# Optimization experiments

Measured on AMD Instinct MI355X. Metric: run time of the kernel, lower is better.

## Reference

```python
import jax, jax.numpy as jnp
import numpy as np

N = 100_000      # nodes
E = 1_600_000    # edges
F_IN = 128       # node_features
H1, H2 = 50, 20  # GCLSTM hidden sizes (fixed in the model)


def _norm_weights(src, dst, w, n):
    # PyG get_laplacian(sym): remove self loops, deg over row, sym-normalize.
    w = jnp.where(src == dst, jnp.zeros_like(w), w)  # remove self-loops (weight 0)
    deg = jax.ops.segment_sum(w, src, num_segments=n)
    deg_safe = jnp.where(deg > 0, deg, jnp.ones_like(deg))
    dis = jnp.where(deg > 0, deg_safe ** -0.5, jnp.zeros_like(deg))
    return dis[src] * w * dis[dst]


def _lhat_matvec(x, src, dst, wn, n):
    # L_hat = 2*L/lambda_max - I with sym norm and lambda_max=2  =>  -D^-1/2 A D^-1/2
    return -jax.ops.segment_sum(wn[:, None] * x[src], dst, num_segments=n)


def _gclstm_cell(x, src, dst, wn, n, Wx, bx, theta, bconv, out_ch):
    # One GCLSTM step with H = C = 0 (the model passes H=C=None).
    H = jnp.zeros((n, out_ch), x.dtype)
    C = jnp.zeros((n, out_ch), x.dtype)
    # ChebConv(H) for all 4 gates: Tx_0 = H, Tx_1 = L_hat @ H   (K = 2)
    Tx = jnp.stack([H, _lhat_matvec(H, src, dst, wn, n)])       # [2, n, out]
    conv = jnp.einsum('knf,gkfo->gno', Tx, theta) + bconv[:, None, :]  # [4, n, out]
    Z = x @ Wx + bx                                              # [n, 4*out], gates i,f,c,o
    zi, zf, zc, zo = jnp.split(Z, 4, axis=-1)
    I = jax.nn.sigmoid(zi + conv[0])
    Fg = jax.nn.sigmoid(zf + conv[1])
    T = jnp.tanh(zc + conv[2])
    C = Fg * C + I * T
    O = jax.nn.sigmoid(zo + conv[3])
    return O * jnp.tanh(C)


def setup_inputs() -> dict:
    key = jax.random.key(0)
    ks = jax.random.split(key, 14)
    s = 0.1  # param init scale
    return {
        'x': jax.random.normal(ks[0], (N, F_IN), jnp.float32),
        'edge_index': jax.random.randint(ks[1], (2, E), 0, N, dtype=jnp.int32),
        'edge_weight': jax.random.uniform(ks[2], (E,), jnp.float32),
        # layer 1: W_x for gates i,f,c,o concatenated, Cheb thetas [gate, K, in, out]
        'Wx1': s * jax.random.normal(ks[3], (F_IN, 4 * H1), jnp.float32),
        'bx1': s * jax.random.normal(ks[4], (4 * H1,), jnp.float32),
        'theta1': s * jax.random.normal(ks[5], (4, 2, H1, H1), jnp.float32),
        'bconv1': s * jax.random.normal(ks[6], (4, H1), jnp.float32),
        # layer 2
        'Wx2': s * jax.random.normal(ks[7], (H1, 4 * H2), jnp.float32),
        'bx2': s * jax.random.normal(ks[8], (4 * H2,), jnp.float32),
        'theta2': s * jax.random.normal(ks[9], (4, 2, H2, H2), jnp.float32),
        'bconv2': s * jax.random.normal(ks[10], (4, H2), jnp.float32),
        # linear head
        'Wl': s * jax.random.normal(ks[11], (H2, 1), jnp.float32),
        'bl': s * jax.random.normal(ks[12], (1,), jnp.float32),
    }


def reference(x, edge_index, edge_weight, Wx1, bx1, theta1, bconv1,
              Wx2, bx2, theta2, bconv2, Wl, bl):
    src, dst = edge_index[0], edge_index[1]
    wn = _norm_weights(src, dst, edge_weight, N)
    h = _gclstm_cell(x, src, dst, wn, N, Wx1, bx1, theta1, bconv1, H1)
    h = _gclstm_cell(h, src, dst, wn, N, Wx2, bx2, theta2, bconv2, H2)
    h = jax.nn.relu(h)
    # F.dropout: identity at inference (deterministic baseline)
    return h @ Wl + bl  # [N, 1]
```

## Files before the change

kernel.cpp:

```cpp
#include <hip/hip_runtime.h>
#include <hip/hip_bf16.h>


#define NODES 100000
#define NTILES 6250

typedef float v4f   __attribute__((ext_vector_type(4)));
typedef float fragC __attribute__((ext_vector_type(4)));
typedef short frag8 __attribute__((ext_vector_type(8)));

#define OFF_B1H 0
#define OFF_B2H 40960
#define OFF_PB1 49152
#define OFF_PB2 49792

__device__ __forceinline__ unsigned short f2bf(float f) {
  unsigned int u = __float_as_uint(f);
  u += 0x7fffu + ((u >> 16) & 1u);
  return (unsigned short)(u >> 16);
}
__device__ __forceinline__ float fsig(float z) {
  float t = __builtin_amdgcn_exp2f(z * -1.44269504088896f);
  return __builtin_amdgcn_rcpf(1.0f + t);
}
__device__ __forceinline__ float ftanh(float z) {
  float t = __builtin_amdgcn_exp2f(z * 2.88539008177793f);
  return 1.0f - 2.0f * __builtin_amdgcn_rcpf(t + 1.0f);
}

union bfu { __hip_bfloat162 h; unsigned int u; };

__device__ __forceinline__ void cvt8(const float* v, frag8& hi, frag8& lo) {
  float lof[8];
#pragma unroll
  for (int p = 0; p < 4; ++p) {
    bfu c; c.h = __float22bfloat162_rn(make_float2(v[2 * p], v[2 * p + 1]));
    hi[2 * p]     = (short)(c.u & 0xffffu);
    hi[2 * p + 1] = (short)(c.u >> 16);
    lof[2 * p]     = v[2 * p]     - __uint_as_float((c.u & 0xffffu) << 16);
    lof[2 * p + 1] = v[2 * p + 1] - __uint_as_float(c.u & 0xffff0000u);
  }
#pragma unroll
  for (int p = 0; p < 4; ++p) {
    bfu c; c.h = __float22bfloat162_rn(make_float2(lof[2 * p], lof[2 * p + 1]));
    lo[2 * p]     = (short)(c.u & 0xffffu);
    lo[2 * p + 1] = (short)(c.u >> 16);
  }
}

__global__ void pack_weights(const float* __restrict__ Wx1, const float* __restrict__ bx1,
                             const float* __restrict__ bconv1,
                             const float* __restrict__ Wx2, const float* __restrict__ bx2,
                             const float* __restrict__ bconv2,
                             unsigned char* __restrict__ ws) {
  const int tid = blockIdx.x * blockDim.x + threadIdx.x;
  const int stride = gridDim.x * blockDim.x;
  unsigned short* B1H = (unsigned short*)(ws + OFF_B1H);
  unsigned short* B2H = (unsigned short*)(ws + OFF_B2H);
  float* PB1 = (float*)(ws + OFF_PB1);
  float* PB2 = (float*)(ws + OFF_PB2);

  for (int idx = tid; idx < 20480; idx += stride) {
    int j = idx & 7, lane = (idx >> 3) & 63, ft = idx >> 9;
    int s = ft / 10, t = ft % 10;
    int k = 32 * s + ((lane >> 4) << 3) + j;
    int m = lane & 15;
    int c = -1, g = 0;
    if (t <= 8) { g = t % 3; c = 16 * (t / 3) + m; }
    else if (m < 6) { c = 48 + m / 3; g = m % 3; }
    float val = 0.f;
    if (c >= 0) {
      int gs = (g == 0) ? 0 : (g == 1) ? 2 : 3;
      val = Wx1[k * 200 + gs * 50 + c];
    }
    B1H[idx] = f2bf(val);
  }
  for (int idx = tid; idx < 4096; idx += stride) {
    int j = idx & 7, lane = (idx >> 3) & 63, ft = idx >> 9;
    int s = ft >> 2, t = ft & 3;
    int k = 32 * s + ((lane >> 4) << 3) + j;
    int m = lane & 15;
    int c = -1, g = 0;
    if (t <= 2) { g = t; c = m; }
    else if (m < 12) { c = 16 + m / 3; g = m % 3; }
    float val = 0.f;
    if (c >= 0 && k < 50) {
      int gs = (g == 0) ? 0 : (g == 1) ? 2 : 3;
      val = Wx2[k * 80 + gs * 20 + c];
    }
    B2H[idx] = f2bf(val);
  }
  for (int idx = tid; idx < 160; idx += stride) {
    int t = idx >> 4, m = idx & 15;
    int c = -1, g = 0;
    if (t <= 8) { g = t % 3; c = 16 * (t / 3) + m; }
    else if (m < 6) { c = 48 + m / 3; g = m % 3; }
    float v = 0.f;
    if (c >= 0) {
      int gs = (g == 0) ? 0 : (g == 1) ? 2 : 3;
      v = bx1[gs * 50 + c] + bconv1[gs * 50 + c];
    }
    PB1[idx] = v;
  }
  for (int idx = tid; idx < 64; idx += stride) {
    int t = idx >> 4, m = idx & 15;
    int c = -1, g = 0;
    if (t <= 2) { g = t; c = m; }
    else if (m < 12) { c = 16 + m / 3; g = m % 3; }
    float v = 0.f;
    if (c >= 0) {
      int gs = (g == 0) ? 0 : (g == 1) ? 2 : 3;
      v = bx2[gs * 20 + c] + bconv2[gs * 20 + c];
    }
    PB2[idx] = v;
  }
}

__global__ __launch_bounds__(256) void gclstm_main(
    const float* __restrict__ x, const unsigned char* __restrict__ wsb,
    const float* __restrict__ Wl, const float* __restrict__ bl,
    float* __restrict__ out) {
  __shared__ short sB1[20480];
  __shared__ unsigned short sH[4][16 * 72];
  __shared__ float sPB1[160];
  __shared__ float sPB2[64];

  const int tid = threadIdx.x;
  const int lane = tid & 63;
  const int wave = tid >> 6;
  const int m = lane & 15;
  const int q = lane >> 4;
  const int tau = blockIdx.x * 4 + wave;

  {
    const v4f* g1 = (const v4f*)(wsb + OFF_B1H);
    v4f* s1 = (v4f*)sB1;
    for (int i = tid; i < 2560; i += 256) s1[i] = g1[i];
    const float* p1 = (const float*)(wsb + OFF_PB1);
    if (tid < 160) sPB1[tid] = p1[tid];
    const float* p2 = (const float*)(wsb + OFF_PB2);
    if (tid < 64) sPB2[tid] = p2[tid];
    unsigned int* hz = (unsigned int*)sH;
    for (int i = tid; i < 2304; i += 256) hz[i] = 0u;
  }
  __syncthreads();

  if (tau >= NTILES) return;

  unsigned short* sHw = (unsigned short*)sH + wave * (16 * 72);
  const frag8* sB1f = (const frag8*)sB1;

  const float* xr = x + (size_t)(tau * 16 + m) * 128 + q * 8;
  v4f xb[8];
#pragma unroll
  for (int s = 0; s < 4; ++s) {
    xb[2 * s] = *(const v4f*)(xr + 32 * s);
    xb[2 * s + 1] = *(const v4f*)(xr + 32 * s + 4);
  }

  fragC acc[10];
#pragma unroll
  for (int t = 0; t < 10; ++t) {
    float bv = sPB1[16 * t + m];
    acc[t] = (fragC){bv, bv, bv, bv};
  }
#pragma unroll
  for (int s = 0; s < 4; ++s) {
    float av[8];
    *(v4f*)av = xb[2 * s];
    *(v4f*)(av + 4) = xb[2 * s + 1];
    frag8 ah, al;
    cvt8(av, ah, al);
#pragma unroll
    for (int t = 0; t < 10; ++t) {
      frag8 b = sB1f[(s * 10 + t) * 64 + lane];
      acc[t] = __builtin_amdgcn_mfma_f32_16x16x32_bf16(ah, b, acc[t], 0, 0, 0);
      acc[t] = __builtin_amdgcn_mfma_f32_16x16x32_bf16(al, b, acc[t], 0, 0, 0);
    }
    __builtin_amdgcn_sched_barrier(0);
  }

#pragma unroll
  for (int b = 0; b < 3; ++b)
#pragma unroll
    for (int r = 0; r < 4; ++r) {
      float I = fsig(acc[3 * b][r]);
      float T = ftanh(acc[3 * b + 1][r]);
      float O = fsig(acc[3 * b + 2][r]);
      sHw[(q * 4 + r) * 72 + 16 * b + m] = f2bf(O * ftanh(I * T));
    }
#pragma unroll
  for (int r = 0; r < 4; ++r) {
    float vI = __shfl(acc[9][r], 16 * q + m);
    float vT = __shfl(acc[9][r], 16 * q + m + 1);
    float vO = __shfl(acc[9][r], 16 * q + m + 2);
    if (m == 0 || m == 3) {
      float I = fsig(vI), T = ftanh(vT), O = fsig(vO);
      sHw[(q * 4 + r) * 72 + 48 + (m >> 1)] = f2bf(O * ftanh(I * T));
    }
  }

  const frag8* g2 = (const frag8*)(wsb + OFF_B2H);
  frag8 hh[2];
#pragma unroll
  for (int s = 0; s < 2; ++s)
    hh[s] = *(const frag8*)(sHw + m * 72 + 32 * s + 8 * q);
  fragC acc2[4];
#pragma unroll
  for (int t = 0; t < 4; ++t) {
    float bv = sPB2[16 * t + m];
    acc2[t] = (fragC){bv, bv, bv, bv};
  }
#pragma unroll
  for (int s = 0; s < 2; ++s)
#pragma unroll
    for (int t = 0; t < 4; ++t) {
      frag8 b = g2[(s * 4 + t) * 64 + lane];
      acc2[t] = __builtin_amdgcn_mfma_f32_16x16x32_bf16(hh[s], b, acc2[t], 0, 0, 0);
    }

  const float wlm = Wl[m];
  const float wlx = (m < 4) ? Wl[16 + m] : 0.f;
  const float blv = bl[0];
  v4f res;
#pragma unroll
  for (int r = 0; r < 4; ++r) {
    float I = fsig(acc2[0][r]);
    float T = ftanh(acc2[1][r]);
    float O = fsig(acc2[2][r]);
    float h2 = O * ftanh(I * T);
    float part = fmaxf(h2, 0.f) * wlm;
    float eI = __shfl(acc2[3][r], 16 * q + 3 * m);
    float eT = __shfl(acc2[3][r], 16 * q + 3 * m + 1);
    float eO = __shfl(acc2[3][r], 16 * q + 3 * m + 2);
    float I2 = fsig(eI), T2 = ftanh(eT), O2 = fsig(eO);
    float h2x = O2 * ftanh(I2 * T2);
    part += fmaxf(h2x, 0.f) * wlx;
    part += __shfl_xor(part, 1);
    part += __shfl_xor(part, 2);
    part += __shfl_xor(part, 4);
    part += __shfl_xor(part, 8);
    res[r] = part + blv;
  }
  if (m == 0) *(v4f*)(out + tau * 16 + 4 * q) = res;
}

extern "C" void kernel_launch(void* const* d_in, const int* in_sizes, int n_in,
                              void* d_out, int out_size, void* d_ws, size_t ws_size,
                              hipStream_t stream) {
  (void)in_sizes; (void)n_in; (void)out_size; (void)ws_size;
  const float* x = (const float*)d_in[0];
  const float* Wx1 = (const float*)d_in[3];
  const float* bx1 = (const float*)d_in[4];
  const float* bconv1 = (const float*)d_in[6];
  const float* Wx2 = (const float*)d_in[7];
  const float* bx2 = (const float*)d_in[8];
  const float* bconv2 = (const float*)d_in[10];
  const float* Wl = (const float*)d_in[11];
  const float* bl = (const float*)d_in[12];
  unsigned char* ws = (unsigned char*)d_ws;

  hipLaunchKernelGGL(pack_weights, dim3(32), dim3(256), 0, stream,
                     Wx1, bx1, bconv1, Wx2, bx2, bconv2, ws);
  hipLaunchKernelGGL(gclstm_main, dim3((NTILES + 3) / 4), dim3(256), 0, stream,
                     x, ws, Wl, bl, (float*)d_out);
}
```

Measured before the change: 134.7 us.

## Read packed layer-1 weights directly from global instead of staging in LDS

```diff
diff --git a/kernel.cpp b/kernel.cpp
--- a/kernel.cpp
+++ b/kernel.cpp
@@ -116,14 +116,11 @@
   }
 }
 
-__global__ __launch_bounds__(256) void gclstm_main(
+__global__ __launch_bounds__(256, 3) void gclstm_main(
     const float* __restrict__ x, const unsigned char* __restrict__ wsb,
     const float* __restrict__ Wl, const float* __restrict__ bl,
     float* __restrict__ out) {
-  __shared__ short sB1[20480];
   __shared__ unsigned short sH[4][16 * 72];
-  __shared__ float sPB1[160];
-  __shared__ float sPB2[64];
 
   const int tid = threadIdx.x;
   const int lane = tid & 63;
@@ -131,24 +128,22 @@
   const int m = lane & 15;
   const int q = lane >> 4;
   const int tau = blockIdx.x * 4 + wave;
+  if (tau >= NTILES) return;
+
+  unsigned short* sHw = (unsigned short*)sH + wave * (16 * 72);
 
   {
-    const v4f* g1 = (const v4f*)(wsb + OFF_B1H);
-    v4f* s1 = (v4f*)sB1;
-    for (int i = tid; i < 2560; i += 256) s1[i] = g1[i];
-    const float* p1 = (const float*)(wsb + OFF_PB1);
-    if (tid < 160) sPB1[tid] = p1[tid];
-    const float* p2 = (const float*)(wsb + OFF_PB2);
-    if (tid < 64) sPB2[tid] = p2[tid];
-    unsigned int* hz = (unsigned int*)sH;
-    for (int i = tid; i < 2304; i += 256) hz[i] = 0u;
-  }
-  __syncthreads();
-
-  if (tau >= NTILES) return;
-
-  unsigned short* sHw = (unsigned short*)sH + wave * (16 * 72);
-  const frag8* sB1f = (const frag8*)sB1;
+    int r0 = lane >> 2, c0 = 48 + (lane & 3) * 4;
+    *(unsigned long long*)(sHw + r0 * 72 + c0) = 0ull;
+  }
+
+  const float* pb1 = (const float*)(wsb + OFF_PB1);
+  const float* pb2 = (const float*)(wsb + OFF_PB2);
+  float bias1v[10], bias2v[4];
+#pragma unroll
+  for (int t = 0; t < 10; ++t) bias1v[t] = pb1[16 * t + m];
+#pragma unroll
+  for (int t = 0; t < 4; ++t) bias2v[t] = pb2[16 * t + m];
 
   const float* xr = x + (size_t)(tau * 16 + m) * 128 + q * 8;
   v4f xb[8];
@@ -158,12 +153,11 @@
     xb[2 * s + 1] = *(const v4f*)(xr + 32 * s + 4);
   }
 
+  const frag8* g1 = (const frag8*)(wsb + OFF_B1H);
   fragC acc[10];
 #pragma unroll
-  for (int t = 0; t < 10; ++t) {
-    float bv = sPB1[16 * t + m];
-    acc[t] = (fragC){bv, bv, bv, bv};
-  }
+  for (int t = 0; t < 10; ++t)
+    acc[t] = (fragC){bias1v[t], bias1v[t], bias1v[t], bias1v[t]};
 #pragma unroll
   for (int s = 0; s < 4; ++s) {
     float av[8];
@@ -173,7 +167,7 @@
     cvt8(av, ah, al);
 #pragma unroll
     for (int t = 0; t < 10; ++t) {
-      frag8 b = sB1f[(s * 10 + t) * 64 + lane];
+      frag8 b = g1[(s * 10 + t) * 64 + lane];
       acc[t] = __builtin_amdgcn_mfma_f32_16x16x32_bf16(ah, b, acc[t], 0, 0, 0);
       acc[t] = __builtin_amdgcn_mfma_f32_16x16x32_bf16(al, b, acc[t], 0, 0, 0);
     }
@@ -207,10 +201,8 @@
     hh[s] = *(const frag8*)(sHw + m * 72 + 32 * s + 8 * q);
   fragC acc2[4];
 #pragma unroll
-  for (int t = 0; t < 4; ++t) {
-    float bv = sPB2[16 * t + m];
-    acc2[t] = (fragC){bv, bv, bv, bv};
-  }
+  for (int t = 0; t < 4; ++t)
+    acc2[t] = (fragC){bias2v[t], bias2v[t], bias2v[t], bias2v[t]};
 #pragma unroll
   for (int s = 0; s < 2; ++s)
 #pragma unroll
```

Result: no change. 132.5 us (-1.6%).
